# Performance work log

Hardware: AMD Instinct MI355X
Metric: run time of the kernel (lower is better)

The kernel has to match this reference:

```python
import jax, jax.numpy as jnp
import numpy as np
from jax import lax

GROUPS = 32
EPS = 1e-5
N_STEPS = 8   # fixed-step stand-in for adaptive implicit_adams
N_CORR = 2    # trapezoidal (Adams-Moulton) corrector iterations


def group_norm(x, gamma, beta):
    B, C, H, W = x.shape
    xg = x.reshape(B, GROUPS, C // GROUPS, H, W)
    mean = xg.mean(axis=(2, 3, 4), keepdims=True)
    var = xg.var(axis=(2, 3, 4), keepdims=True)
    xg = (xg - mean) * lax.rsqrt(var + EPS)
    return xg.reshape(B, C, H, W) * gamma[None, :, None, None] + beta[None, :, None, None]


def batch_norm1d(x, gamma, beta):  # training-mode batch stats, x: [B,C,L]
    mean = x.mean(axis=(0, 2), keepdims=True)
    var = x.var(axis=(0, 2), keepdims=True)
    return (x - mean) * lax.rsqrt(var + EPS) * gamma[None, :, None] + beta[None, :, None]


def conv1d(x, w, b):  # x [B,Cin,L], w [Cout,Cin,3], pad=1
    y = lax.conv_general_dilated(x, w, (1,), [(1, 1)], dimension_numbers=('NCH', 'OIH', 'NCH'))
    return y + b[None, :, None]


def concat_conv2d(t, x, w, b):  # x [B,C,H,W], w [C, C+1, 3,3], pad=1
    tt = jnp.full_like(x[:, :1], t)
    ttx = jnp.concatenate([tt, x], axis=1)
    y = lax.conv_general_dilated(ttx, w, (1, 1), [(1, 1), (1, 1)], dimension_numbers=('NCHW', 'OIHW', 'NCHW'))
    return y + b[None, :, None, None]


def make_odefunc(cw1, cb1, gn1_g, gn1_b, gn2_g, gn2_b, cw2, cb2, gn3_g, gn3_b):
    def f(t, x):
        out = jax.nn.relu(group_norm(x, gn1_g, gn1_b))
        out = concat_conv2d(t, out, cw1, cb1)
        out = jax.nn.elu(group_norm(out, gn2_g, gn2_b))
        out = concat_conv2d(t, out, cw2, cb2)
        return group_norm(out, gn3_g, gn3_b)
    return f


def ode_integrate(f, y0):
    h = 1.0 / N_STEPS

    def step(y, i):
        t = i.astype(y.dtype) * h
        f0 = f(t, y)
        y1 = y + h * f0  # explicit predictor
        for _ in range(N_CORR):  # implicit (trapezoidal AM) corrector
            y1 = y + 0.5 * h * (f0 + f(t + h, y1))
        return y1, None

    yT, _ = lax.scan(step, y0, jnp.arange(N_STEPS))
    return yT


def setup_inputs() -> dict:
    key = jax.random.key(0)
    ks = jax.random.split(key, 8)
    B, L, C = 16, 4096, 256
    inp = {
        'x': jax.random.normal(ks[0], (B, 4, 1, L), dtype=jnp.float32),
        'w1': jax.random.normal(ks[1], (64, 4, 3), dtype=jnp.float32) * 0.1,
        'b1': jnp.zeros((64,), jnp.float32),
        'bn1_g': jnp.ones((64,), jnp.float32), 'bn1_b': jnp.zeros((64,), jnp.float32),
        'w2': jax.random.normal(ks[2], (256, 64, 3), dtype=jnp.float32) * 0.05,
        'b2': jnp.zeros((256,), jnp.float32),
        'bn2_g': jnp.ones((256,), jnp.float32), 'bn2_b': jnp.zeros((256,), jnp.float32),
        'cw1': jax.random.normal(ks[3], (C, C + 1, 3, 3), dtype=jnp.float32) * 0.02,
        'cb1': jnp.zeros((C,), jnp.float32),
        'gn1_g': jnp.ones((C,), jnp.float32), 'gn1_b': jnp.zeros((C,), jnp.float32),
        'gn2_g': jnp.ones((C,), jnp.float32), 'gn2_b': jnp.zeros((C,), jnp.float32),
        'cw2': jax.random.normal(ks[4], (C, C + 1, 3, 3), dtype=jnp.float32) * 0.02,
        'cb2': jnp.zeros((C,), jnp.float32),
        'gn3_g': jnp.ones((C,), jnp.float32), 'gn3_b': jnp.zeros((C,), jnp.float32),
    }
    return inp


def reference(x, w1, b1, bn1_g, bn1_b, w2, b2, bn2_g, bn2_b,
              cw1, cb1, gn1_g, gn1_b, gn2_g, gn2_b, cw2, cb2, gn3_g, gn3_b):
    h = x[:, :, 0, :]                       # squeeze(2) -> [B,4,L]
    h = jax.nn.relu(batch_norm1d(conv1d(h, w1, b1), bn1_g, bn1_b))
    h = jnp.tanh(batch_norm1d(conv1d(h, w2, b2), bn2_g, bn2_b))
    y0 = h[:, :, None, :]                   # unsqueeze(2) -> [B,256,1,L]
    f = make_odefunc(cw1, cb1, gn1_g, gn1_b, gn2_g, gn2_b, cw2, cb2, gn3_g, gn3_b)
    return ode_integrate(f, y0)
```

## Files before the change

kernel.cpp:

```cpp
#include <hip/hip_runtime.h>
#include <math.h>

#define L4 4096

typedef short bf16x8 __attribute__((ext_vector_type(8)));
typedef float f32x4 __attribute__((ext_vector_type(4)));

__device__ __forceinline__ unsigned short f2bf(float f) {
  unsigned u = __builtin_bit_cast(unsigned, f);
  return (unsigned short)((u + 0x7FFFu + ((u >> 16) & 1u)) >> 16);
}
__device__ __forceinline__ float bf2f(unsigned short h) {
  unsigned u = ((unsigned)h) << 16;
  return __builtin_bit_cast(float, u);
}

__global__ __launch_bounds__(256) void pack_big(const float* __restrict__ cw,
                                                unsigned short* __restrict__ Apack,
                                                float* __restrict__ Tpack) {
  int gid = blockIdx.x * 256 + threadIdx.x;
  if (gid < 768) {
    int o = gid & 255, tap = gid >> 8;
    Tpack[tap * 256 + o] = cw[((size_t)o * 257) * 9 + 3 + tap];
  }
  if (gid >= 16 * 24 * 64) return;
  int frow = gid / 1536;
  int rem = gid - frow * 1536;
  int ks = rem >> 6;
  int lane = rem & 63;
  int o = frow * 16 + (lane & 15);
  int tap = ks >> 3;
  int ib = ((ks & 7) << 5) + ((lane >> 4) << 3);
#pragma unroll
  for (int e = 0; e < 8; e++) {
    int i = ib + e;
    Apack[(size_t)gid * 8 + e] = f2bf(cw[((size_t)o * 257 + (i + 1)) * 9 + 3 + tap]);
  }
}

__global__ __launch_bounds__(256) void pack_stem(const float* __restrict__ w2,
                                                 unsigned short* __restrict__ Apack) {
  int gid = blockIdx.x * 256 + threadIdx.x;
  if (gid >= 16 * 6 * 64) return;
  int frow = gid / 384;
  int rem = gid - frow * 384;
  int ks = rem >> 6;
  int lane = rem & 63;
  int o = frow * 16 + (lane & 15);
  int tap = ks >> 1;
  int ib = ((ks & 1) << 5) + ((lane >> 4) << 3);
#pragma unroll
  for (int e = 0; e < 8; e++) {
    int i = ib + e;
    Apack[(size_t)gid * 8 + e] = f2bf(w2[((size_t)o * 64 + i) * 3 + tap]);
  }
}

__global__ __launch_bounds__(256) void conv1_kernel(const float* __restrict__ x,
                                                    const float* __restrict__ w,
                                                    const float* __restrict__ bias,
                                                    unsigned short* __restrict__ out) {
  int idx = blockIdx.x * 256 + threadIdx.x;
  int l = idx & 4095;
  int c = (idx >> 12) & 63;
  int b = idx >> 18;
  const float* xb = x + (size_t)b * 4 * L4;
  const float* wc = w + c * 12;
  float acc = bias[c];
#pragma unroll
  for (int i = 0; i < 4; i++) {
    float x0 = (l > 0) ? xb[i * L4 + l - 1] : 0.f;
    float x1 = xb[i * L4 + l];
    float x2 = (l < 4095) ? xb[i * L4 + l + 1] : 0.f;
    acc += wc[i * 3] * x0 + wc[i * 3 + 1] * x1 + wc[i * 3 + 2] * x2;
  }
  out[idx] = f2bf(acc);
}

__global__ __launch_bounds__(256) void stats_kernel(const float* __restrict__ in,
                                                    float* __restrict__ stats,
                                                    int unit_stride, int nrow,
                                                    int row_stride, int rowlen,
                                                    float inv_n) {
  int u = blockIdx.x;
  const float* base = in + (size_t)u * unit_stride;
  float s = 0.f, s2 = 0.f;
  for (int r = 0; r < nrow; r++) {
    const float* rowp = base + (size_t)r * row_stride;
    for (int j = threadIdx.x * 4; j < rowlen; j += 256 * 4) {
      float4 v = *(const float4*)(rowp + j);
      s += v.x + v.y + v.z + v.w;
      s2 += v.x * v.x + v.y * v.y + v.z * v.z + v.w * v.w;
    }
  }
  __shared__ float sh[512];
  sh[threadIdx.x] = s;
  sh[256 + threadIdx.x] = s2;
  __syncthreads();
  for (int off = 128; off > 0; off >>= 1) {
    if (threadIdx.x < off) {
      sh[threadIdx.x] += sh[threadIdx.x + off];
      sh[256 + threadIdx.x] += sh[256 + threadIdx.x + off];
    }
    __syncthreads();
  }
  if (threadIdx.x == 0) {
    float m = sh[0] * inv_n;
    float var = sh[256] * inv_n - m * m;
    stats[u * 2] = m;
    stats[u * 2 + 1] = rsqrtf(var + 1e-5f);
  }
}

__global__ __launch_bounds__(256) void stats_bf16_kernel(const unsigned short* __restrict__ in,
                                                         float* __restrict__ stats,
                                                         int unit_stride, int nrow,
                                                         int row_stride, int rowlen,
                                                         float inv_n) {
  int u = blockIdx.x;
  const unsigned short* base = in + (size_t)u * unit_stride;
  float s = 0.f, s2 = 0.f;
  for (int r = 0; r < nrow; r++) {
    const unsigned short* rowp = base + (size_t)r * row_stride;
    for (int j = threadIdx.x * 4; j < rowlen; j += 256 * 4) {
      ushort4 v = *(const ushort4*)(rowp + j);
      float va = bf2f(v.x), vb = bf2f(v.y), vc = bf2f(v.z), vd = bf2f(v.w);
      s += va + vb + vc + vd;
      s2 += va * va + vb * vb + vc * vc + vd * vd;
    }
  }
  __shared__ float sh[512];
  sh[threadIdx.x] = s;
  sh[256 + threadIdx.x] = s2;
  __syncthreads();
  for (int off = 128; off > 0; off >>= 1) {
    if (threadIdx.x < off) {
      sh[threadIdx.x] += sh[threadIdx.x + off];
      sh[256 + threadIdx.x] += sh[256 + threadIdx.x + off];
    }
    __syncthreads();
  }
  if (threadIdx.x == 0) {
    float m = sh[0] * inv_n;
    float var = sh[256] * inv_n - m * m;
    stats[u * 2] = m;
    stats[u * 2 + 1] = rsqrtf(var + 1e-5f);
  }
}

__global__ __launch_bounds__(256) void act_transpose64(const unsigned short* __restrict__ inv,
                                                       const float* __restrict__ stats,
                                                       const float* __restrict__ gamma,
                                                       const float* __restrict__ beta,
                                                       unsigned short* __restrict__ Xt) {
  constexpr int C = 64;
  __shared__ unsigned short tile[64 * C];
  int bidx = blockIdx.x;
  int b = bidx >> 6;
  int lt = bidx & 63;
  int l0 = lt << 6;
  int t = threadIdx.x;
  int lanel = t & 63;
  int cq = t >> 6;
  for (int cp = 0; cp < C / 4; cp++) {
    int c = cp * 4 + cq;
    float m = stats[2 * c], rs = stats[2 * c + 1];
    float ga = gamma[c] * rs, be = beta[c] - m * ga;
    size_t gidx = ((size_t)b * C + c) * 4096 + l0 + lanel;
    float v = bf2f(inv[gidx]);
    float a = v * ga + be;
    float r = fmaxf(a, 0.f);
    int sw = (lanel & 15) << 2;
    tile[lanel * C + (c ^ sw)] = f2bf(r);
  }
  __syncthreads();
  constexpr int CH = C / 4;
  constexpr int RPP = 256 / CH;
  for (int p = 0; p < 64 / RPP; p++) {
    int r = p * RPP + t / CH;
    int ch = t % CH;
    int sw = (r & 15) << 2;
    ushort4 v = *(const ushort4*)&tile[r * C + ((ch * 4) ^ sw)];
    *(ushort4*)&Xt[((size_t)b * 4098 + 1 + l0 + r) * C + ch * 4] = v;
  }
  if (lt == 0) {
    if (t < C / 4) *(ushort4*)&Xt[((size_t)b * 4098 + 0) * C + t * 4] = make_ushort4(0, 0, 0, 0);
  } else if (lt == 63) {
    if (t < C / 4) *(ushort4*)&Xt[((size_t)b * 4098 + 4097) * C + t * 4] = make_ushort4(0, 0, 0, 0);
  }
}

template <int NKS, int KLG, int CIN, int NORM, int ACT, int NCH, bool INBF, bool TCH, int OUT>
__global__ __launch_bounds__(512, 4) void gemm_T(const void* __restrict__ Bsrc,
                                                 const unsigned short* __restrict__ Apack,
                                                 const float* __restrict__ Pin,
                                                 const float* __restrict__ gng,
                                                 const float* __restrict__ gnb,
                                                 const float* __restrict__ Tpack,
                                                 const float* __restrict__ bias,
                                                 float tval,
                                                 void* __restrict__ outv,
                                                 float* __restrict__ Pout) {
  constexpr int CPR = CIN / 8;
  constexpr int CPRLG = (CIN == 256) ? 5 : 3;
  constexpr int ROWS = 66;
  constexpr int RPI = 512 >> CPRLG;
  __shared__ unsigned short bsm[ROWS * CIN];
  __shared__ float gsm[32][2];
  __shared__ float ebias[256];
  __shared__ float psh[32][2];

  int tid = threadIdx.x;
  int lane = tid & 63;
  int wv = tid >> 6;
  int b = blockIdx.x >> 6;
  int lt = blockIdx.x & 63;
  int l_base = lt << 6;
  int wo0 = wv << 5;
  int col = lane & 15;
  int grp = lane >> 4;

  if (NORM) {
    int g = tid >> 4, j0 = tid & 15;
    const float* Pg = Pin + ((size_t)b * 32 + g) * 128;
    float s = 0.f, s2 = 0.f;
    for (int j = j0; j < NCH; j += 16) { s += Pg[j * 2]; s2 += Pg[j * 2 + 1]; }
#pragma unroll
    for (int off = 8; off; off >>= 1) { s += __shfl_down(s, off, 16); s2 += __shfl_down(s2, off, 16); }
    if (j0 == 0) {
      float m = s * (1.f / 32768.f);
      float var = s2 * (1.f / 32768.f) - m * m;
      gsm[g][0] = m;
      gsm[g][1] = rsqrtf(var + 1e-5f);
    }
  }
  if (tid < 256) {
    float e = bias[tid];
    if (TCH) e += tval * (Tpack[tid] + Tpack[256 + tid] + Tpack[512 + tid]);
    ebias[tid] = e;
  }
  if (OUT == 0 && tid >= 256 && tid < 288) { psh[tid - 256][0] = 0.f; psh[tid - 256][1] = 0.f; }
  __syncthreads();

  {
    int pl = tid & (CPR - 1);
    int rowbase = tid >> CPRLG;
    float ga[8], be[8];
    if (NORM) {
      float m = gsm[pl][0], rs = gsm[pl][1];
      float4 g0 = *(const float4*)&gng[pl * 8];
      float4 g1 = *(const float4*)&gng[pl * 8 + 4];
      float4 b0 = *(const float4*)&gnb[pl * 8];
      float4 b1 = *(const float4*)&gnb[pl * 8 + 4];
      const float* gp = &g0.x;
      const float* bp = &b0.x;
      ga[0] = g0.x * rs; ga[1] = g0.y * rs; ga[2] = g0.z * rs; ga[3] = g0.w * rs;
      ga[4] = g1.x * rs; ga[5] = g1.y * rs; ga[6] = g1.z * rs; ga[7] = g1.w * rs;
      be[0] = b0.x - m * ga[0]; be[1] = b0.y - m * ga[1];
      be[2] = b0.z - m * ga[2]; be[3] = b0.w - m * ga[3];
      be[4] = b1.x - m * ga[4]; be[5] = b1.y - m * ga[5];
      be[6] = b1.z - m * ga[6]; be[7] = b1.w - m * ga[7];
      (void)gp; (void)bp;
    }
#pragma unroll
    for (int it = 0; it < (ROWS + RPI - 1) / RPI; it++) {
      int row = rowbase + it * RPI;
      if (row < ROWS) {
        int wchunk = (row << CPRLG) | (pl ^ (row & 7));
        bf16x8 o8;
        if (NORM) {
          int gl = l_base - 1 + row;
          if (gl >= 0 && gl < 4096) {
            size_t base = ((size_t)b * 4096 + gl) * CIN + pl * 8;
            float vv[8];
            if (INBF) {
              bf16x8 raw = *(const bf16x8*)((const unsigned short*)Bsrc + base);
#pragma unroll
              for (int e = 0; e < 8; e++) vv[e] = bf2f((unsigned short)raw[e]);
            } else {
              float4 r0 = *(const float4*)((const float*)Bsrc + base);
              float4 r1 = *(const float4*)((const float*)Bsrc + base + 4);
              vv[0] = r0.x; vv[1] = r0.y; vv[2] = r0.z; vv[3] = r0.w;
              vv[4] = r1.x; vv[5] = r1.y; vv[6] = r1.z; vv[7] = r1.w;
            }
#pragma unroll
            for (int e = 0; e < 8; e++) {
              float a = vv[e] * ga[e] + be[e];
              float r = (ACT == 0) ? fmaxf(a, 0.f) : (a > 0.f ? a : expm1f(a));
              o8[e] = (short)f2bf(r);
            }
          } else {
            o8 = (bf16x8){0, 0, 0, 0, 0, 0, 0, 0};
          }
        } else {
          o8 = *(const bf16x8*)((const unsigned short*)Bsrc +
                                ((size_t)b * 4098 + l_base + row) * CIN + pl * 8);
        }
        *(bf16x8*)&bsm[(size_t)wchunk * 8] = o8;
      }
    }
  }
  __syncthreads();

  const unsigned short* apk = Apack + ((size_t)(wv * 2) * NKS) * 512 + (size_t)lane * 8;

  f32x4 acc[2][4];
#pragma unroll
  for (int i = 0; i < 2; i++)
#pragma unroll
    for (int j = 0; j < 4; j++) acc[i][j] = (f32x4){0.f, 0.f, 0.f, 0.f};

#pragma unroll 2
  for (int ks = 0; ks < NKS; ks++) {
    int tap = ks >> KLG;
    int cbase = (ks & ((1 << KLG) - 1)) << 2;
    bf16x8 bfr[4], afr[2];
#pragma unroll
    for (int fc = 0; fc < 4; fc++) {
      int lr = col + fc * 16 + tap;
      int cb = (cbase + grp) ^ (lr & 7);
      bfr[fc] = *(const bf16x8*)&bsm[((size_t)(lr << CPRLG) + cb) * 8];
    }
#pragma unroll
    for (int fo = 0; fo < 2; fo++)
      afr[fo] = *(const bf16x8*)(apk + ((size_t)fo * NKS + ks) * 512);
#pragma unroll
    for (int fo = 0; fo < 2; fo++)
#pragma unroll
      for (int fc = 0; fc < 4; fc++)
        acc[fo][fc] = __builtin_amdgcn_mfma_f32_16x16x32_bf16(afr[fo], bfr[fc], acc[fo][fc], 0, 0, 0);
  }

  float ps = 0.f, ps2 = 0.f;
#pragma unroll
  for (int fo = 0; fo < 2; fo++) {
    int o0 = wo0 + fo * 16 + grp * 4;
    float eb[4], w0c[4], w2c[4];
#pragma unroll
    for (int r = 0; r < 4; r++) { eb[r] = ebias[o0 + r]; w0c[r] = 0.f; w2c[r] = 0.f; }
    if (TCH && lt == 0) {
#pragma unroll
      for (int r = 0; r < 4; r++) w0c[r] = tval * Tpack[o0 + r];
    }
    if (TCH && lt == 63) {
#pragma unroll
      for (int r = 0; r < 4; r++) w2c[r] = tval * Tpack[512 + o0 + r];
    }
#pragma unroll
    for (int fc = 0; fc < 4; fc++) {
      int l = l_base + fc * 16 + col;
      float v[4];
#pragma unroll
      for (int r = 0; r < 4; r++) {
        v[r] = acc[fo][fc][r] + eb[r];
        if (TCH) {
          if (lt == 0) v[r] -= (l == 0) ? w0c[r] : 0.f;
          if (lt == 63) v[r] -= (l == 4095) ? w2c[r] : 0.f;
        }
        if (OUT == 0) { ps += v[r]; ps2 += v[r] * v[r]; }
      }
      if (OUT == 0) {
        ushort4 pk;
        pk.x = f2bf(v[0]); pk.y = f2bf(v[1]); pk.z = f2bf(v[2]); pk.w = f2bf(v[3]);
        *(ushort4*)((unsigned short*)outv + ((size_t)b * 4096 + l) * 256 + o0) = pk;
      } else {
#pragma unroll
        for (int r = 0; r < 4; r++)
          ((float*)outv)[((size_t)b * 256 + o0 + r) * 4096 + l] = v[r];
      }
    }
    if (OUT == 0) {
      float s = ps, s2 = ps2;
#pragma unroll
      for (int off = 8; off; off >>= 1) {
        s += __shfl_down(s, off, 16);
        s2 += __shfl_down(s2, off, 16);
      }
      if (col == 0) {
        int g = wv * 4 + fo * 2 + (grp >> 1);
        atomicAdd(&psh[g][0], s);
        atomicAdd(&psh[g][1], s2);
      }
      ps = 0.f; ps2 = 0.f;
    }
  }

  if (OUT == 0) {
    __syncthreads();
    if (tid < 32) {
      size_t pi = ((size_t)b * 32 + tid) * 128 + (size_t)lt * 2;
      Pout[pi] = psh[tid][0];
      Pout[pi + 1] = psh[tid][1];
    }
  }
}

__global__ __launch_bounds__(512) void bn_tanh_T(const float* __restrict__ Q,
                                                 const float* __restrict__ stats,
                                                 const float* __restrict__ gamma,
                                                 const float* __restrict__ beta,
                                                 float* __restrict__ Y,
                                                 float* __restrict__ P1) {
  int tid = threadIdx.x;
  int b = blockIdx.x >> 5;
  int seg = blockIdx.x & 31;
  int c = tid >> 1;
  float m = stats[2 * c], rs = stats[2 * c + 1];
  float ga = gamma[c] * rs, be = beta[c] - m * ga;
  __shared__ float psh[32][2];
  if (tid < 32) { psh[tid][0] = 0.f; psh[tid][1] = 0.f; }
  __syncthreads();
  float s = 0.f, s2 = 0.f;
  for (int it = 0; it < 16; it++) {
    int l4 = (tid & 1) + it * 2;
    int l0 = seg * 128 + l4 * 4;
    float4 v = *(const float4*)&Q[((size_t)b * 256 + c) * 4096 + l0];
    float r0 = tanhf(v.x * ga + be);
    float r1 = tanhf(v.y * ga + be);
    float r2 = tanhf(v.z * ga + be);
    float r3 = tanhf(v.w * ga + be);
    Y[((size_t)b * 4096 + l0 + 0) * 256 + c] = r0;
    Y[((size_t)b * 4096 + l0 + 1) * 256 + c] = r1;
    Y[((size_t)b * 4096 + l0 + 2) * 256 + c] = r2;
    Y[((size_t)b * 4096 + l0 + 3) * 256 + c] = r3;
    s += r0 + r1 + r2 + r3;
    s2 += r0 * r0 + r1 * r1 + r2 * r2 + r3 * r3;
  }
#pragma unroll
  for (int off = 8; off; off >>= 1) { s += __shfl_down(s, off, 16); s2 += __shfl_down(s2, off, 16); }
  if ((tid & 15) == 0) {
    int g = c >> 3;
    atomicAdd(&psh[g][0], s);
    atomicAdd(&psh[g][1], s2);
  }
  __syncthreads();
  if (tid < 32) {
    size_t pi = ((size_t)b * 32 + tid) * 128 + (size_t)seg * 2;
    P1[pi] = psh[tid][0];
    P1[pi + 1] = psh[tid][1];
  }
}

template <int MODE>
__global__ __launch_bounds__(512) void combine_T(const unsigned short* __restrict__ F,
                                                 const float* __restrict__ P3,
                                                 const float* __restrict__ gng,
                                                 const float* __restrict__ gnb,
                                                 float* __restrict__ Y,
                                                 unsigned short* __restrict__ Y1,
                                                 float* __restrict__ P1) {
  __shared__ float gsm[32][2];
  __shared__ float gabe[256][2];
  __shared__ float psh[32][2];
  int tid = threadIdx.x;
  int b = blockIdx.x >> 5;
  int seg = blockIdx.x & 31;
  {
    int g = tid >> 4, j0 = tid & 15;
    const float* Pg = P3 + ((size_t)b * 32 + g) * 128;
    float s = 0.f, s2 = 0.f;
    for (int j = j0; j < 64; j += 16) { s += Pg[j * 2]; s2 += Pg[j * 2 + 1]; }
#pragma unroll
    for (int off = 8; off; off >>= 1) { s += __shfl_down(s, off, 16); s2 += __shfl_down(s2, off, 16); }
    if (j0 == 0) {
      float m = s * (1.f / 32768.f);
      float var = s2 * (1.f / 32768.f) - m * m;
      gsm[g][0] = m;
      gsm[g][1] = rsqrtf(var + 1e-5f);
    }
  }
  __syncthreads();
  if (tid < 256) {
    float m = gsm[tid >> 3][0], rs = gsm[tid >> 3][1];
    float ga = gng[tid] * rs;
    gabe[tid][0] = ga;
    gabe[tid][1] = gnb[tid] - m * ga;
  }
  if (tid >= 256 && tid < 288) { psh[tid - 256][0] = 0.f; psh[tid - 256][1] = 0.f; }
  __syncthreads();

  size_t base4 = ((size_t)b * 4096 + seg * 128) * 64;
  int c0 = (tid << 2) & 255;
  int g = c0 >> 3;
  float ga0 = gabe[c0][0], be0 = gabe[c0][1];
  float ga1 = gabe[c0 + 1][0], be1 = gabe[c0 + 1][1];
  float ga2 = gabe[c0 + 2][0], be2 = gabe[c0 + 2][1];
  float ga3 = gabe[c0 + 3][0], be3 = gabe[c0 + 3][1];
  float s = 0.f, s2 = 0.f;
  for (int i = tid; i < 8192; i += 512) {
    size_t idx4 = base4 + i;
    ushort4 fv = ((const ushort4*)F)[idx4];
    float4 yv = ((const float4*)Y)[idx4];
    float f0 = bf2f(fv.x) * ga0 + be0;
    float f1 = bf2f(fv.y) * ga1 + be1;
    float f2 = bf2f(fv.z) * ga2 + be2;
    float f3 = bf2f(fv.w) * ga3 + be3;
    float4 yn;
    yn.x = yv.x + (MODE == 0 ? 0.125f : 0.0625f) * f0;
    yn.y = yv.y + (MODE == 0 ? 0.125f : 0.0625f) * f1;
    yn.z = yv.z + (MODE == 0 ? 0.125f : 0.0625f) * f2;
    yn.w = yv.w + (MODE == 0 ? 0.125f : 0.0625f) * f3;
    if (MODE == 0) {
      float4 yb;
      yb.x = yv.x + 0.0625f * f0;
      yb.y = yv.y + 0.0625f * f1;
      yb.z = yv.z + 0.0625f * f2;
      yb.w = yv.w + 0.0625f * f3;
      ((float4*)Y)[idx4] = yb;
    }
    if (MODE == 2) {
      ((float4*)Y)[idx4] = yn;
    } else {
      ushort4 pk;
      pk.x = f2bf(yn.x); pk.y = f2bf(yn.y); pk.z = f2bf(yn.z); pk.w = f2bf(yn.w);
      ((ushort4*)Y1)[idx4] = pk;
    }
    s += yn.x + yn.y + yn.z + yn.w;
    s2 += yn.x * yn.x + yn.y * yn.y + yn.z * yn.z + yn.w * yn.w;
  }
  s += __shfl_xor(s, 1);
  s2 += __shfl_xor(s2, 1);
  if ((tid & 1) == 0) {
    atomicAdd(&psh[g][0], s);
    atomicAdd(&psh[g][1], s2);
  }
  __syncthreads();
  if (tid < 32) {
    size_t pi = ((size_t)b * 32 + tid) * 128 + (size_t)seg * 2;
    P1[pi] = psh[tid][0];
    P1[pi + 1] = psh[tid][1];
  }
}

__global__ __launch_bounds__(256) void transpose_final(const float* __restrict__ Y,
                                                       float* __restrict__ out) {
  __shared__ float tile[64 * 260];
  int b = blockIdx.x >> 6;
  int lt = blockIdx.x & 63;
  int t = threadIdx.x;
  for (int i = t; i < 4096; i += 256) {
    int r = i >> 6;
    int c4 = (i & 63) << 2;
    float4 v = *(const float4*)&Y[((size_t)b * 4096 + lt * 64 + r) * 256 + c4];
    *(float4*)&tile[r * 260 + c4] = v;
  }
  __syncthreads();
  for (int i = t; i < 4096; i += 256) {
    int c = i >> 4;
    int l4 = (i & 15) << 2;
    float4 v;
    v.x = tile[(l4 + 0) * 260 + c];
    v.y = tile[(l4 + 1) * 260 + c];
    v.z = tile[(l4 + 2) * 260 + c];
    v.w = tile[(l4 + 3) * 260 + c];
    *(float4*)&out[((size_t)b * 256 + c) * 4096 + lt * 64 + l4] = v;
  }
}

extern "C" void kernel_launch(void* const* d_in, const int* in_sizes, int n_in,
                              void* d_out, int out_size, void* d_ws, size_t ws_size,
                              hipStream_t stream) {
  const float* x = (const float*)d_in[0];
  const float* w1 = (const float*)d_in[1];
  const float* b1 = (const float*)d_in[2];
  const float* bn1_g = (const float*)d_in[3];
  const float* bn1_b = (const float*)d_in[4];
  const float* w2 = (const float*)d_in[5];
  const float* b2 = (const float*)d_in[6];
  const float* bn2_g = (const float*)d_in[7];
  const float* bn2_b = (const float*)d_in[8];
  const float* cw1 = (const float*)d_in[9];
  const float* cb1 = (const float*)d_in[10];
  const float* gn1_g = (const float*)d_in[11];
  const float* gn1_b = (const float*)d_in[12];
  const float* gn2_g = (const float*)d_in[13];
  const float* gn2_b = (const float*)d_in[14];
  const float* cw2 = (const float*)d_in[15];
  const float* cb2 = (const float*)d_in[16];
  const float* gn3_g = (const float*)d_in[17];
  const float* gn3_b = (const float*)d_in[18];

  const size_t SZ = (size_t)16 * 256 * 4096;

  char* p = (char*)d_ws;
  float* Ybuf = (float*)p;                   p += SZ * 4;
  unsigned short* C1 = (unsigned short*)p;   p += SZ * 2;
  unsigned short* Fb = (unsigned short*)p;   p += SZ * 2;
  unsigned short* APK1 = (unsigned short*)p; p += (size_t)16 * 24 * 64 * 8 * 2;
  unsigned short* APK2 = (unsigned short*)p; p += (size_t)16 * 24 * 64 * 8 * 2;
  unsigned short* APKS = (unsigned short*)p; p += (size_t)16 * 6 * 64 * 8 * 2;
  float* TP1 = (float*)p;                    p += 768 * 4;
  float* TP2 = (float*)p;                    p += 768 * 4;
  float* STATS = (float*)p;                  p += 1024 * 4;
  float* P1 = (float*)p;                     p += (size_t)16 * 32 * 128 * 4;
  float* P2 = (float*)p;                     p += (size_t)16 * 32 * 128 * 4;
  float* P3 = (float*)p;                     p += (size_t)16 * 32 * 128 * 4;

  float* Q = (float*)d_out;
  unsigned short* Y1 = (unsigned short*)d_out;

  pack_big<<<96, 256, 0, stream>>>(cw1, APK1, TP1);
  pack_big<<<96, 256, 0, stream>>>(cw2, APK2, TP2);
  pack_stem<<<24, 256, 0, stream>>>(w2, APKS);

  conv1_kernel<<<16384, 256, 0, stream>>>(x, w1, b1, C1);
  stats_bf16_kernel<<<64, 256, 0, stream>>>(C1, STATS, 4096, 16, 64 * 4096, 4096, 1.f / 65536.f);
  act_transpose64<<<1024, 256, 0, stream>>>(C1, STATS, bn1_g, bn1_b, Fb);
  gemm_T<6, 1, 64, 0, 0, 32, true, false, 1><<<1024, 512, 0, stream>>>(
      Fb, APKS, nullptr, nullptr, nullptr, nullptr, b2, 0.f, Q, nullptr);
  stats_kernel<<<256, 256, 0, stream>>>(Q, STATS, 4096, 16, 256 * 4096, 4096, 1.f / 65536.f);
  bn_tanh_T<<<512, 512, 0, stream>>>(Q, STATS, bn2_g, bn2_b, Ybuf, P1);

  const float H = 0.125f;
  for (int i = 0; i < 8; i++) {
    float t = i * H;
    gemm_T<24, 3, 256, 1, 0, 32, false, true, 0><<<1024, 512, 0, stream>>>(
        Ybuf, APK1, P1, gn1_g, gn1_b, TP1, cb1, t, C1, P2);
    gemm_T<24, 3, 256, 1, 1, 64, true, true, 0><<<1024, 512, 0, stream>>>(
        C1, APK2, P2, gn2_g, gn2_b, TP2, cb2, t, Fb, P3);
    combine_T<0><<<512, 512, 0, stream>>>(Fb, P3, gn3_g, gn3_b, Ybuf, Y1, P1);
    for (int c = 0; c < 2; c++) {
      gemm_T<24, 3, 256, 1, 0, 32, true, true, 0><<<1024, 512, 0, stream>>>(
          Y1, APK1, P1, gn1_g, gn1_b, TP1, cb1, t + H, C1, P2);
      gemm_T<24, 3, 256, 1, 1, 64, true, true, 0><<<1024, 512, 0, stream>>>(
          C1, APK2, P2, gn2_g, gn2_b, TP2, cb2, t + H, Fb, P3);
      if (c == 0)
        combine_T<1><<<512, 512, 0, stream>>>(Fb, P3, gn3_g, gn3_b, Ybuf, Y1, P1);
      else
        combine_T<2><<<512, 512, 0, stream>>>(Fb, P3, gn3_g, gn3_b, Ybuf, Y1, P1);
    }
  }

  transpose_final<<<1024, 256, 0, stream>>>(Ybuf, (float*)d_out);
}
```

Baseline: 2.650 ms.

## Reorder packed weights by k-step, linearize LDS staging, use packed bf16 converts

Packed A weights are re-laid out k-step-major so that all waves read contiguous memory for each k-step. LDS staging writes linear chunks and moves the XOR swizzle onto the global-read side. The GEMM k-loop is fully unrolled with hoisted LDS base addresses. Scalar bf16 rounding is replaced by the v_cvt_pk_bf16_f32 instruction, and tanh/expm1 are replaced by fast exp-based approximations, which may change precision slightly.

```diff
diff --git a/kernel.cpp b/kernel.cpp
--- a/kernel.cpp
+++ b/kernel.cpp
@@ -13,6 +13,15 @@
 __device__ __forceinline__ float bf2f(unsigned short h) {
   unsigned u = ((unsigned)h) << 16;
   return __builtin_bit_cast(float, u);
+}
+__device__ __forceinline__ unsigned pk2(float lo, float hi) {
+  unsigned d;
+  asm("v_cvt_pk_bf16_f32 %0, %1, %2" : "=v"(d) : "v"(lo), "v"(hi));
+  return d;
+}
+__device__ __forceinline__ float fast_tanh(float x) {
+  float e = __expf(2.f * x);
+  return 1.f - 2.f * __builtin_amdgcn_rcpf(e + 1.f);
 }
 
 __global__ __launch_bounds__(256) void pack_big(const float* __restrict__ cw,
@@ -23,11 +32,10 @@
     int o = gid & 255, tap = gid >> 8;
     Tpack[tap * 256 + o] = cw[((size_t)o * 257) * 9 + 3 + tap];
   }
-  if (gid >= 16 * 24 * 64) return;
-  int frow = gid / 1536;
-  int rem = gid - frow * 1536;
-  int ks = rem >> 6;
-  int lane = rem & 63;
+  if (gid >= 24 * 16 * 64) return;
+  int ks = gid >> 10;
+  int frow = (gid >> 6) & 15;
+  int lane = gid & 63;
   int o = frow * 16 + (lane & 15);
   int tap = ks >> 3;
   int ib = ((ks & 7) << 5) + ((lane >> 4) << 3);
@@ -41,11 +49,10 @@
 __global__ __launch_bounds__(256) void pack_stem(const float* __restrict__ w2,
                                                  unsigned short* __restrict__ Apack) {
   int gid = blockIdx.x * 256 + threadIdx.x;
-  if (gid >= 16 * 6 * 64) return;
-  int frow = gid / 384;
-  int rem = gid - frow * 384;
-  int ks = rem >> 6;
-  int lane = rem & 63;
+  if (gid >= 6 * 16 * 64) return;
+  int ks = gid >> 10;
+  int frow = (gid >> 6) & 15;
+  int lane = gid & 63;
   int o = frow * 16 + (lane & 15);
   int tap = ks >> 1;
   int ib = ((ks & 1) << 5) + ((lane >> 4) << 3);
@@ -205,6 +212,7 @@
   constexpr int CPRLG = (CIN == 256) ? 5 : 3;
   constexpr int ROWS = 66;
   constexpr int RPI = 512 >> CPRLG;
+  constexpr int TOT = ROWS * CPR;
   __shared__ unsigned short bsm[ROWS * CIN];
   __shared__ float gsm[32][2];
   __shared__ float ebias[256];
@@ -244,34 +252,32 @@
 
   {
     int pl = tid & (CPR - 1);
-    int rowbase = tid >> CPRLG;
+    int row0 = tid >> CPRLG;
+    int gch = pl ^ (row0 & 7);
     float ga[8], be[8];
     if (NORM) {
-      float m = gsm[pl][0], rs = gsm[pl][1];
-      float4 g0 = *(const float4*)&gng[pl * 8];
-      float4 g1 = *(const float4*)&gng[pl * 8 + 4];
-      float4 b0 = *(const float4*)&gnb[pl * 8];
-      float4 b1 = *(const float4*)&gnb[pl * 8 + 4];
-      const float* gp = &g0.x;
-      const float* bp = &b0.x;
+      float m = gsm[gch][0], rs = gsm[gch][1];
+      float4 g0 = *(const float4*)&gng[gch * 8];
+      float4 g1 = *(const float4*)&gng[gch * 8 + 4];
+      float4 b0 = *(const float4*)&gnb[gch * 8];
+      float4 b1 = *(const float4*)&gnb[gch * 8 + 4];
       ga[0] = g0.x * rs; ga[1] = g0.y * rs; ga[2] = g0.z * rs; ga[3] = g0.w * rs;
       ga[4] = g1.x * rs; ga[5] = g1.y * rs; ga[6] = g1.z * rs; ga[7] = g1.w * rs;
       be[0] = b0.x - m * ga[0]; be[1] = b0.y - m * ga[1];
       be[2] = b0.z - m * ga[2]; be[3] = b0.w - m * ga[3];
       be[4] = b1.x - m * ga[4]; be[5] = b1.y - m * ga[5];
       be[6] = b1.z - m * ga[6]; be[7] = b1.w - m * ga[7];
-      (void)gp; (void)bp;
-    }
-#pragma unroll
-    for (int it = 0; it < (ROWS + RPI - 1) / RPI; it++) {
-      int row = rowbase + it * RPI;
-      if (row < ROWS) {
-        int wchunk = (row << CPRLG) | (pl ^ (row & 7));
-        bf16x8 o8;
+    }
+#pragma unroll
+    for (int it = 0; it < (TOT + 511) / 512; it++) {
+      int chunk = it * 512 + tid;
+      if (chunk < TOT) {
+        int row = row0 + it * RPI;
+        uint4 w4;
         if (NORM) {
           int gl = l_base - 1 + row;
           if (gl >= 0 && gl < 4096) {
-            size_t base = ((size_t)b * 4096 + gl) * CIN + pl * 8;
+            size_t base = ((size_t)b * 4096 + gl) * CIN + gch * 8;
             float vv[8];
             if (INBF) {
               bf16x8 raw = *(const bf16x8*)((const unsigned short*)Bsrc + base);
@@ -283,26 +289,28 @@
               vv[0] = r0.x; vv[1] = r0.y; vv[2] = r0.z; vv[3] = r0.w;
               vv[4] = r1.x; vv[5] = r1.y; vv[6] = r1.z; vv[7] = r1.w;
             }
+            float rr[8];
 #pragma unroll
             for (int e = 0; e < 8; e++) {
               float a = vv[e] * ga[e] + be[e];
-              float r = (ACT == 0) ? fmaxf(a, 0.f) : (a > 0.f ? a : expm1f(a));
-              o8[e] = (short)f2bf(r);
+              rr[e] = (ACT == 0) ? fmaxf(a, 0.f) : (a > 0.f ? a : __expf(a) - 1.f);
             }
+            w4.x = pk2(rr[0], rr[1]); w4.y = pk2(rr[2], rr[3]);
+            w4.z = pk2(rr[4], rr[5]); w4.w = pk2(rr[6], rr[7]);
           } else {
-            o8 = (bf16x8){0, 0, 0, 0, 0, 0, 0, 0};
+            w4 = make_uint4(0, 0, 0, 0);
           }
         } else {
-          o8 = *(const bf16x8*)((const unsigned short*)Bsrc +
-                                ((size_t)b * 4098 + l_base + row) * CIN + pl * 8);
+          w4 = *(const uint4*)((const unsigned short*)Bsrc +
+                               ((size_t)b * 4098 + l_base + row) * CIN + gch * 8);
         }
-        *(bf16x8*)&bsm[(size_t)wchunk * 8] = o8;
+        *(uint4*)&bsm[(size_t)chunk * 8] = w4;
       }
     }
   }
   __syncthreads();
 
-  const unsigned short* apk = Apack + ((size_t)(wv * 2) * NKS) * 512 + (size_t)lane * 8;
+  const unsigned short* apk = Apack + (size_t)(wv * 2) * 512 + (size_t)lane * 8;
 
   f32x4 acc[2][4];
 #pragma unroll
@@ -310,20 +318,19 @@
 #pragma unroll
     for (int j = 0; j < 4; j++) acc[i][j] = (f32x4){0.f, 0.f, 0.f, 0.f};
 
-#pragma unroll 2
+#pragma unroll
   for (int ks = 0; ks < NKS; ks++) {
     int tap = ks >> KLG;
     int cbase = (ks & ((1 << KLG) - 1)) << 2;
+    int lr0 = col + tap;
+    int cb = (cbase + grp) ^ (lr0 & 7);
+    const unsigned short* bp = &bsm[((size_t)(lr0 << CPRLG) + cb) * 8];
+    const unsigned short* ap = apk + (size_t)ks * 16 * 512;
     bf16x8 bfr[4], afr[2];
 #pragma unroll
-    for (int fc = 0; fc < 4; fc++) {
-      int lr = col + fc * 16 + tap;
-      int cb = (cbase + grp) ^ (lr & 7);
-      bfr[fc] = *(const bf16x8*)&bsm[((size_t)(lr << CPRLG) + cb) * 8];
-    }
-#pragma unroll
-    for (int fo = 0; fo < 2; fo++)
-      afr[fo] = *(const bf16x8*)(apk + ((size_t)fo * NKS + ks) * 512);
+    for (int fc = 0; fc < 4; fc++) bfr[fc] = *(const bf16x8*)(bp + fc * 16 * CIN);
+#pragma unroll
+    for (int fo = 0; fo < 2; fo++) afr[fo] = *(const bf16x8*)(ap + fo * 512);
 #pragma unroll
     for (int fo = 0; fo < 2; fo++)
 #pragma unroll
@@ -360,9 +367,8 @@
         if (OUT == 0) { ps += v[r]; ps2 += v[r] * v[r]; }
       }
       if (OUT == 0) {
-        ushort4 pk;
-        pk.x = f2bf(v[0]); pk.y = f2bf(v[1]); pk.z = f2bf(v[2]); pk.w = f2bf(v[3]);
-        *(ushort4*)((unsigned short*)outv + ((size_t)b * 4096 + l) * 256 + o0) = pk;
+        uint2 pk = make_uint2(pk2(v[0], v[1]), pk2(v[2], v[3]));
+        *(uint2*)((unsigned short*)outv + ((size_t)b * 4096 + l) * 256 + o0) = pk;
       } else {
 #pragma unroll
         for (int r = 0; r < 4; r++)
@@ -415,10 +421,10 @@
     int l4 = (tid & 1) + it * 2;
     int l0 = seg * 128 + l4 * 4;
     float4 v = *(const float4*)&Q[((size_t)b * 256 + c) * 4096 + l0];
-    float r0 = tanhf(v.x * ga + be);
-    float r1 = tanhf(v.y * ga + be);
-    float r2 = tanhf(v.z * ga + be);
-    float r3 = tanhf(v.w * ga + be);
+    float r0 = fast_tanh(v.x * ga + be);
+    float r1 = fast_tanh(v.y * ga + be);
+    float r2 = fast_tanh(v.z * ga + be);
+    float r3 = fast_tanh(v.w * ga + be);
     Y[((size_t)b * 4096 + l0 + 0) * 256 + c] = r0;
     Y[((size_t)b * 4096 + l0 + 1) * 256 + c] = r1;
     Y[((size_t)b * 4096 + l0 + 2) * 256 + c] = r2;
@@ -511,9 +517,8 @@
     if (MODE == 2) {
       ((float4*)Y)[idx4] = yn;
     } else {
-      ushort4 pk;
-      pk.x = f2bf(yn.x); pk.y = f2bf(yn.y); pk.z = f2bf(yn.z); pk.w = f2bf(yn.w);
-      ((ushort4*)Y1)[idx4] = pk;
+      uint2 pk = make_uint2(pk2(yn.x, yn.y), pk2(yn.z, yn.w));
+      ((uint2*)Y1)[idx4] = pk;
     }
     s += yn.x + yn.y + yn.z + yn.w;
     s2 += yn.x * yn.x + yn.y * yn.y + yn.z * yn.z + yn.w * yn.w;
@@ -586,9 +591,9 @@
   float* Ybuf = (float*)p;                   p += SZ * 4;
   unsigned short* C1 = (unsigned short*)p;   p += SZ * 2;
   unsigned short* Fb = (unsigned short*)p;   p += SZ * 2;
-  unsigned short* APK1 = (unsigned short*)p; p += (size_t)16 * 24 * 64 * 8 * 2;
-  unsigned short* APK2 = (unsigned short*)p; p += (size_t)16 * 24 * 64 * 8 * 2;
-  unsigned short* APKS = (unsigned short*)p; p += (size_t)16 * 6 * 64 * 8 * 2;
+  unsigned short* APK1 = (unsigned short*)p; p += (size_t)24 * 16 * 64 * 8 * 2;
+  unsigned short* APK2 = (unsigned short*)p; p += (size_t)24 * 16 * 64 * 8 * 2;
+  unsigned short* APKS = (unsigned short*)p; p += (size_t)6 * 16 * 64 * 8 * 2;
   float* TP1 = (float*)p;                    p += 768 * 4;
   float* TP2 = (float*)p;                    p += 768 * 4;
   float* STATS = (float*)p;                  p += 1024 * 4;
```

Measured after the change: 2.617 ms. No clear change (-1.2%).
